# Performance work log

Hardware: AMD Instinct MI355X
Metric: run time of the kernel (lower is better)

Reference implementation:

```python
import jax, jax.numpy as jnp
import numpy as np

D = 1024      # d_model
H = 16        # n_head
DH = D // H   # d_head = 64
DFF = 4 * D   # 4096
B, T = 1, 4096
EPS = 1e-5


def _layernorm(x, scale, bias):
    mu = jnp.mean(x, axis=-1, keepdims=True)
    var = jnp.mean(jnp.square(x - mu), axis=-1, keepdims=True)
    return (x - mu) * jax.lax.rsqrt(var + EPS) * scale + bias


def setup_inputs() -> dict:
    key = jax.random.key(0)
    ks = jax.random.split(key, 8)
    s = 0.02
    return {
        "x": jax.random.normal(ks[0], (B, T, D), jnp.float32),
        "ln1_scale": jnp.ones((D,), jnp.float32),
        "ln1_bias": jnp.zeros((D,), jnp.float32),
        "W_attn": jax.random.normal(ks[1], (D, 3 * D), jnp.float32) * s,
        "b_attn": jnp.zeros((3 * D,), jnp.float32),
        "W_proj": jax.random.normal(ks[2], (D, D), jnp.float32) * s,
        "b_proj": jnp.zeros((D,), jnp.float32),
        "ln2_scale": jnp.ones((D,), jnp.float32),
        "ln2_bias": jnp.zeros((D,), jnp.float32),
        "W_fc": jax.random.normal(ks[3], (D, DFF), jnp.float32) * s,
        "b_fc": jnp.zeros((DFF,), jnp.float32),
        "W_fc2": jax.random.normal(ks[4], (DFF, D), jnp.float32) * s,
        "b_fc2": jnp.zeros((D,), jnp.float32),
    }


def reference(x, ln1_scale, ln1_bias, W_attn, b_attn, W_proj, b_proj,
              ln2_scale, ln2_bias, W_fc, b_fc, W_fc2, b_fc2):
    Bx, Tx, C = x.shape
    # --- attention branch ---
    h = _layernorm(x, ln1_scale, ln1_bias)
    qkv = h @ W_attn + b_attn                      # [B,T,3D]
    q, k, v = jnp.split(qkv, 3, axis=-1)
    q = q.reshape(Bx, Tx, H, DH).transpose(0, 2, 1, 3)  # [B,H,T,dh]
    k = k.reshape(Bx, Tx, H, DH).transpose(0, 2, 1, 3)
    v = v.reshape(Bx, Tx, H, DH).transpose(0, 2, 1, 3)
    att = jnp.einsum('bhqd,bhkd->bhqk', q, k) * (1.0 / jnp.sqrt(DH))
    causal = jnp.tril(jnp.ones((Tx, Tx), dtype=jnp.bool_))[None, None]
    att = jnp.where(causal, att, -jnp.inf)
    att = jax.nn.softmax(att, axis=-1)
    y = jnp.einsum('bhqk,bhkd->bhqd', att, v)      # [B,H,T,dh]
    y = y.transpose(0, 2, 1, 3).reshape(Bx, Tx, C)
    y = y @ W_proj + b_proj
    x = x + y
    # --- MLP branch ---
    h2 = _layernorm(x, ln2_scale, ln2_bias)
    m = jax.nn.gelu(h2 @ W_fc + b_fc)              # approximate gelu (flax default)
    m = m @ W_fc2 + b_fc2
    return x + m
```

## Files before the change

### kernel.cpp

```cpp
#include <hip/hip_runtime.h>
#include <hip/hip_bf16.h>

typedef short bf16x8 __attribute__((ext_vector_type(8)));
typedef float f32x4 __attribute__((ext_vector_type(4)));
typedef unsigned short u16;
typedef unsigned int u32;

#define TSEQ 4096
#define DMODEL 1024
#define NHEAD 16
#define DHEAD 64
#define DFF 4096

__device__ __forceinline__ u16 f2bf(float f) {
    u32 u = __builtin_bit_cast(u32, f);
    u32 lsb = (u >> 16) & 1u;
    u += 0x7fffu + lsb;
    return (u16)(u >> 16);
}

__device__ __forceinline__ float exp2_hw(float x) {
    float r;
    asm("v_exp_f32 %0, %1" : "=v"(r) : "v"(x));
    return r;
}

__device__ __forceinline__ float rcp_hw(float x) {
    float r;
    asm("v_rcp_f32 %0, %1" : "=v"(r) : "v"(x));
    return r;
}

__device__ __forceinline__ u32 cvt_pk_bf16(float a, float b) {
    u32 r;
    asm("v_cvt_pk_bf16_f32 %0, %1, %2" : "=v"(r) : "v"(a), "v"(b));
    return r;
}

__device__ __forceinline__ void gload_lds16(const u16* g, u16* l) {
    __builtin_amdgcn_global_load_lds(
        (const __attribute__((address_space(1))) u32*)g,
        (__attribute__((address_space(3))) u32*)l, 16, 0, 0);
}

__global__ __launch_bounds__(256)
void transpose_cast_kernel(const float* __restrict__ W, u16* __restrict__ Wt, int K, int N)
{
    __shared__ float tile[64][65];
    const int t = threadIdx.x;
    const int c = t & 63, r4 = t >> 6;
    const int col0 = blockIdx.x * 64;
    const int row0 = blockIdx.y * 64;
#pragma unroll
    for (int p = 0; p < 16; p++) {
        const int r = 4 * p + r4;
        tile[r][c] = W[(size_t)(row0 + r) * N + col0 + c];
    }
    __syncthreads();
#pragma unroll
    for (int p = 0; p < 16; p++) {
        const int r = 4 * p + r4;
        Wt[(size_t)(col0 + r) * K + row0 + c] = f2bf(tile[c][r]);
    }
}

__global__ __launch_bounds__(256)
void v_transpose_kernel(const u16* __restrict__ qkv, u16* __restrict__ Vtg)
{
    __shared__ u16 tile[64][72];
    const int t = threadIdx.x;
    const int hh = blockIdx.y, t0 = blockIdx.x * 64;
#pragma unroll
    for (int p = 0; p < 2; p++) {
        const int L = p * 2048 + t * 8;
        const int r = L >> 6, c = L & 63;
        const bf16x8 v = *(const bf16x8*)(qkv + (size_t)(t0 + r) * 3072 + 2048 + hh * 64 + c);
#pragma unroll
        for (int i = 0; i < 8; i++) tile[c + i][r] = (u16)v[i];
    }
    __syncthreads();
#pragma unroll
    for (int p = 0; p < 2; p++) {
        const int L = p * 2048 + t * 8;
        const int d = L >> 6, c = L & 63;
        bf16x8 v;
#pragma unroll
        for (int i = 0; i < 8; i++) v[i] = (short)tile[d][c + i];
        *(bf16x8*)(Vtg + (size_t)(hh * 64 + d) * TSEQ + t0 + c) = v;
    }
}

__global__ __launch_bounds__(256)
void ln_kernel(const float* __restrict__ x, const float* __restrict__ sc,
               const float* __restrict__ bi, u16* __restrict__ out)
{
    const int lane = threadIdx.x & 63;
    const int row = blockIdx.x * 4 + (threadIdx.x >> 6);
    const float* xr = x + (size_t)row * DMODEL;
    float4 v[4];
    float s = 0.f, s2 = 0.f;
#pragma unroll
    for (int q = 0; q < 4; q++) {
        v[q] = *(const float4*)(xr + 4 * (lane + 64 * q));
        s  += v[q].x + v[q].y + v[q].z + v[q].w;
        s2 += v[q].x * v[q].x + v[q].y * v[q].y + v[q].z * v[q].z + v[q].w * v[q].w;
    }
#pragma unroll
    for (int off = 1; off < 64; off <<= 1) {
        s  += __shfl_xor(s, off);
        s2 += __shfl_xor(s2, off);
    }
    const float mu = s * (1.f / DMODEL);
    const float rstd = rsqrtf(s2 * (1.f / DMODEL) - mu * mu + 1e-5f);
#pragma unroll
    for (int q = 0; q < 4; q++) {
        const int c = 4 * (lane + 64 * q);
        const float4 scv = *(const float4*)(sc + c);
        const float4 biv = *(const float4*)(bi + c);
        ushort4 ov;
        ov.x = f2bf((v[q].x - mu) * rstd * scv.x + biv.x);
        ov.y = f2bf((v[q].y - mu) * rstd * scv.y + biv.y);
        ov.z = f2bf((v[q].z - mu) * rstd * scv.z + biv.z);
        ov.w = f2bf((v[q].w - mu) * rstd * scv.w + biv.w);
        *(ushort4*)(out + (size_t)row * DMODEL + c) = ov;
    }
}

template<int BN, int GELU_F, int OUT_BF16, int HAS_RES, int HAS_BIAS, int FUSE_Z1 = 0>
__global__ __launch_bounds__(256)
void gemm_kernel(const u16* __restrict__ A, int lda,
                 const u16* __restrict__ Bt, int ldb,
                 const float* __restrict__ bias, const float* __restrict__ res,
                 u16* __restrict__ outb, float* __restrict__ outf0,
                 float* __restrict__ outf1, int M, int N, int Kblk)
{
    constexpr int MI = (BN == 128) ? 4 : 2;
    __shared__ u16 Alds[128 * 64];
    __shared__ u16 Blds[BN * 64];
    const int t = threadIdx.x;
    const int lane = t & 63, w = t >> 6;
    const int g = lane >> 4, fr = lane & 15;
    const int m0 = blockIdx.y * 128, n0 = blockIdx.x * BN;
    const size_t koff = (size_t)blockIdx.z * Kblk;
    const int rowbase = (BN == 128) ? (w >> 1) * 64 : w * 32;
    const int colbase = (BN == 128) ? (w & 1) * 64 : 0;
    float* outf = blockIdx.z ? outf1 : outf0;

    f32x4 zero4 = {0.f, 0.f, 0.f, 0.f};
    f32x4 acc[MI][4];
#pragma unroll
    for (int i = 0; i < MI; i++)
#pragma unroll
        for (int j = 0; j < 4; j++) acc[i][j] = zero4;

    for (int k0 = 0; k0 < Kblk; k0 += 64) {
        __syncthreads();
#pragma unroll
        for (int p = 0; p < 4; p++) {
            const int c = p * 256 + t;
            const int r = c >> 3, j = (c & 7) ^ (r & 7);
            gload_lds16(A + (size_t)(m0 + r) * lda + koff + k0 + j * 8, Alds + c * 8);
        }
#pragma unroll
        for (int p = 0; p < (BN == 128 ? 4 : 2); p++) {
            const int c = p * 256 + t;
            const int r = c >> 3, j = (c & 7) ^ (r & 7);
            gload_lds16(Bt + (size_t)(n0 + r) * ldb + koff + k0 + j * 8, Blds + c * 8);
        }
        __syncthreads();

#pragma unroll
        for (int ks = 0; ks < 2; ks++) {
            bf16x8 af[MI], bfr[4];
#pragma unroll
            for (int i = 0; i < MI; i++)
                af[i] = *(const bf16x8*)(Alds + (rowbase + i * 16 + fr) * 64 + (((ks * 4 + g) ^ (fr & 7)) * 8));
#pragma unroll
            for (int j = 0; j < 4; j++)
                bfr[j] = *(const bf16x8*)(Blds + (colbase + j * 16 + fr) * 64 + (((ks * 4 + g) ^ (fr & 7)) * 8));
#pragma unroll
            for (int i = 0; i < MI; i++)
#pragma unroll
                for (int j = 0; j < 4; j++)
                    acc[i][j] = __builtin_amdgcn_mfma_f32_16x16x32_bf16(af[i], bfr[j], acc[i][j], 0, 0, 0);
        }
    }

    const bool fuse = FUSE_Z1 && (blockIdx.z == 1);
#pragma unroll
    for (int j = 0; j < 4; j++) {
        const int col = n0 + colbase + j * 16 + fr;
        float bv = 0.f;
        if (HAS_BIAS) bv = bias[col];
        if (FUSE_Z1 && fuse) bv = bias[col];
#pragma unroll
        for (int i = 0; i < MI; i++) {
#pragma unroll
            for (int r = 0; r < 4; r++) {
                const int row = m0 + rowbase + i * 16 + g * 4 + r;
                float v = acc[i][j][r] + bv;
                if (GELU_F) {
                    const float q = 0.7978845608028654f * (v + 0.044715f * v * v * v);
                    const float e = exp2_hw(fminf(q, 30.f) * 2.8853900817779268f);
                    v = v * e * rcp_hw(e + 1.0f);
                }
                if (HAS_RES) v += res[(size_t)row * N + col];
                if (FUSE_Z1 && fuse) v += res[(size_t)row * N + col];
                if (OUT_BF16) outb[(size_t)row * N + col] = f2bf(v);
                else          outf[(size_t)row * N + col] = v;
            }
        }
    }
}

__global__ __launch_bounds__(256)
void fc2_merge_kernel(float* __restrict__ out, const float* __restrict__ part)
{
    const int i = blockIdx.x * 256 + threadIdx.x;
    const float4 o = ((const float4*)out)[i];
    const float4 p = ((const float4*)part)[i];
    float4 v;
    v.x = o.x + p.x;
    v.y = o.y + p.y;
    v.z = o.z + p.z;
    v.w = o.w + p.w;
    ((float4*)out)[i] = v;
}

__device__ __forceinline__ void softmax_update(
    const f32x4 st[4], bool diag, int klim, int g, int fr,
    float& mrow, float& lrow, f32x4 o[4], u16* Pl)
{
    const float ninf = -__builtin_inff();
    const float C = 0.125f * 1.4426950408889634f;
    float av[4][4];
#pragma unroll
    for (int ct = 0; ct < 4; ct++)
#pragma unroll
        for (int r = 0; r < 4; r++) {
            float aa = st[ct][r];
            if (diag && (ct * 16 + g * 4 + r) > klim) aa = ninf;
            av[ct][r] = aa;
        }
    float m0 = fmaxf(fmaxf(av[0][0], av[0][1]), fmaxf(av[0][2], av[0][3]));
    float m1 = fmaxf(fmaxf(av[1][0], av[1][1]), fmaxf(av[1][2], av[1][3]));
    float m2 = fmaxf(fmaxf(av[2][0], av[2][1]), fmaxf(av[2][2], av[2][3]));
    float m3 = fmaxf(fmaxf(av[3][0], av[3][1]), fmaxf(av[3][2], av[3][3]));
    float vm = fmaxf(fmaxf(m0, m1), fmaxf(m2, m3));
    vm = fmaxf(vm, __shfl_xor(vm, 16));
    vm = fmaxf(vm, __shfl_xor(vm, 32));
    const float mn = (vm <= mrow + 64.f) ? mrow : vm;
    const float mnC = mn * C;
    float rs = 0.f;
#pragma unroll
    for (int ct = 0; ct < 4; ct++) {
        const float p0 = exp2_hw(__builtin_fmaf(av[ct][0], C, -mnC));
        const float p1 = exp2_hw(__builtin_fmaf(av[ct][1], C, -mnC));
        const float p2 = exp2_hw(__builtin_fmaf(av[ct][2], C, -mnC));
        const float p3 = exp2_hw(__builtin_fmaf(av[ct][3], C, -mnC));
        rs += (p0 + p1) + (p2 + p3);
        uint2 pk;
        pk.x = cvt_pk_bf16(p0, p1);
        pk.y = cvt_pk_bf16(p2, p3);
        const int chunk = ct * 2 + (g >> 1);
        const int addr = fr * 64 + ((chunk ^ (fr & 7)) * 8) + (g & 1) * 4;
        *(uint2*)(Pl + addr) = pk;
    }
    rs += __shfl_xor(rs, 16);
    rs += __shfl_xor(rs, 32);
    const float sc = exp2_hw((mrow - mn) * C);
    lrow = __builtin_fmaf(lrow, sc, rs);
    const bool nores = (mn == mrow);
    mrow = mn;
    if (!__all(nores)) {
        float scb[4];
#pragma unroll
        for (int j = 0; j < 4; j++) scb[j] = __shfl(sc, g * 4 + j);
#pragma unroll
        for (int dt = 0; dt < 4; dt++)
#pragma unroll
            for (int j = 0; j < 4; j++) o[dt][j] *= scb[j];
    }
}

__global__ __launch_bounds__(512, 4)
void attn_kernel(const u16* __restrict__ qkv, const u16* __restrict__ Vtg,
                 u16* __restrict__ y)
{
    __shared__ u16 Klds[2][128 * 64];
    __shared__ u16 Vlds[2][64 * 128];
    __shared__ u16 Plds[8][16 * 64];
    const int t = threadIdx.x, lane = t & 63, w = t >> 6;
    const int g = lane >> 4, fr = lane & 15;
    const int wv = w & 3, grp = w >> 2;
    const int hh = blockIdx.y;
    const int ii = blockIdx.x;
    const int ntB = 64 - ii;
    const int qAw = ii * 64 + wv * 16;
    const int qBw = (63 - ii) * 64 + wv * 16;

    bf16x8 aqA[2], aqB[2];
#pragma unroll
    for (int s = 0; s < 2; s++) {
        aqA[s] = *(const bf16x8*)(qkv + (size_t)(qAw + fr) * 3072 + hh * 64 + s * 32 + g * 8);
        aqB[s] = *(const bf16x8*)(qkv + (size_t)(qBw + fr) * 3072 + hh * 64 + s * 32 + g * 8);
    }

    f32x4 zero4 = {0.f, 0.f, 0.f, 0.f};
    f32x4 oA[4] = {zero4, zero4, zero4, zero4};
    f32x4 oB[4] = {zero4, zero4, zero4, zero4};
    const float ninf = -__builtin_inff();
    float mA = ninf, lA = 0.f, mB = ninf, lB = 0.f;

    const int cK0 = t, cK1 = t + 512;
    const int rK0 = cK0 >> 3, jK0 = (cK0 & 7) ^ (rK0 & 7);
    const int rK1 = cK1 >> 3, jK1 = (cK1 & 7) ^ (rK1 & 7);
    const int rv0 = cK0 >> 4, cj0 = cK0 & 15;
    const int jv0 = (cj0 & 8) | ((cj0 & 7) ^ (rv0 & 7));
    const int rv1 = cK1 >> 4, cj1 = cK1 & 15;
    const int jv1 = (cj1 & 8) | ((cj1 & 7) ^ (rv1 & 7));
    const u16* gk0 = qkv + (size_t)rK0 * 3072 + 1024 + hh * 64 + jK0 * 8;
    const u16* gk1 = qkv + (size_t)rK1 * 3072 + 1024 + hh * 64 + jK1 * 8;
    const u16* gv0 = Vtg + (size_t)(hh * 64 + rv0) * TSEQ + jv0 * 8;
    const u16* gv1 = Vtg + (size_t)(hh * 64 + rv1) * TSEQ + jv1 * 8;

#define STAGE(buf, k0) do { \
        gload_lds16(gk0 + (size_t)(k0) * 3072, Klds[buf] + cK0 * 8); \
        gload_lds16(gk1 + (size_t)(k0) * 3072, Klds[buf] + cK1 * 8); \
        gload_lds16(gv0 + (k0), Vlds[buf] + cK0 * 8); \
        gload_lds16(gv1 + (k0), Vlds[buf] + cK1 * 8); \
    } while (0)

    const int nIter = (65 - ii) >> 1;
    STAGE(0, 0);

    int cur = 0;
    for (int j = 0; j < nIter; j++) {
        __syncthreads();
        if (j + 1 < nIter) STAGE(cur ^ 1, (j + 1) * 128);

        const int kt = 2 * j + grp;
        const bool aB = kt < ntB;
        const bool aA = kt <= ii;
        if (aB | aA) {
            const u16* Kl = Klds[cur] + grp * (64 * 64);
            const u16* Vl = Vlds[cur];
            const int klim = wv * 16 + fr;

            f32x4 stA[4] = {zero4, zero4, zero4, zero4};
            f32x4 stB[4] = {zero4, zero4, zero4, zero4};
#pragma unroll
            for (int ct = 0; ct < 4; ct++) {
#pragma unroll
                for (int ds = 0; ds < 2; ds++) {
                    const bf16x8 bk = *(const bf16x8*)(Kl + (ct * 16 + fr) * 64 + (((ds * 4 + g) ^ (fr & 7)) * 8));
                    if (aB) stB[ct] = __builtin_amdgcn_mfma_f32_16x16x32_bf16(bk, aqB[ds], stB[ct], 0, 0, 0);
                    if (aA) stA[ct] = __builtin_amdgcn_mfma_f32_16x16x32_bf16(bk, aqA[ds], stA[ct], 0, 0, 0);
                }
            }

            if (aB) {
                softmax_update(stB, kt == ntB - 1, klim, g, fr, mB, lB, oB, Plds[w]);
                __builtin_amdgcn_s_waitcnt(0xc07f);
#pragma unroll
                for (int kkh = 0; kkh < 2; kkh++) {
                    const bf16x8 pa = *(const bf16x8*)(&Plds[w][fr * 64 + (((kkh * 4 + g) ^ (fr & 7)) * 8)]);
#pragma unroll
                    for (int dt = 0; dt < 4; dt++) {
                        const int cc = grp * 8 + kkh * 4 + g;
                        const bf16x8 bv = *(const bf16x8*)(Vl + (dt * 16 + fr) * 128 + (((cc & 8) | ((cc & 7) ^ (fr & 7))) * 8));
                        oB[dt] = __builtin_amdgcn_mfma_f32_16x16x32_bf16(pa, bv, oB[dt], 0, 0, 0);
                    }
                }
            }
            if (aA) {
                softmax_update(stA, kt == ii, klim, g, fr, mA, lA, oA, Plds[w]);
                __builtin_amdgcn_s_waitcnt(0xc07f);
#pragma unroll
                for (int kkh = 0; kkh < 2; kkh++) {
                    const bf16x8 pa = *(const bf16x8*)(&Plds[w][fr * 64 + (((kkh * 4 + g) ^ (fr & 7)) * 8)]);
#pragma unroll
                    for (int dt = 0; dt < 4; dt++) {
                        const int cc = grp * 8 + kkh * 4 + g;
                        const bf16x8 bv = *(const bf16x8*)(Vl + (dt * 16 + fr) * 128 + (((cc & 8) | ((cc & 7) ^ (fr & 7))) * 8));
                        oA[dt] = __builtin_amdgcn_mfma_f32_16x16x32_bf16(pa, bv, oA[dt], 0, 0, 0);
                    }
                }
            }
        }
        cur ^= 1;
    }
#undef STAGE

    __syncthreads();
    float* Of = (float*)&Klds[0][0];
    float2* Ml = (float2*)&Vlds[0][0];
    const float C = 0.125f * 1.4426950408889634f;
    if (grp == 1) {
#pragma unroll
        for (int dt = 0; dt < 4; dt++)
#pragma unroll
            for (int jq = 0; jq < 4; jq++) {
                Of[((wv * 2 + 0) * 16 + g * 4 + jq) * 64 + dt * 16 + fr] = oA[dt][jq];
                Of[((wv * 2 + 1) * 16 + g * 4 + jq) * 64 + dt * 16 + fr] = oB[dt][jq];
            }
        if (g == 0) {
            Ml[(wv * 2 + 0) * 16 + fr] = make_float2(mA, lA);
            Ml[(wv * 2 + 1) * 16 + fr] = make_float2(mB, lB);
        }
    }
    __syncthreads();
    if (grp == 0) {
#pragma unroll
        for (int jq = 0; jq < 4; jq++) {
            {
                const float m0 = __shfl(mA, g * 4 + jq), l0 = __shfl(lA, g * 4 + jq);
                const float2 ml1 = Ml[(wv * 2 + 0) * 16 + g * 4 + jq];
                const float mm = fmaxf(m0, ml1.x);
                const float s0 = exp2_hw((m0 - mm) * C);
                const float s1 = exp2_hw((ml1.x - mm) * C);
                const float rl = rcp_hw(__builtin_fmaf(l0, s0, ml1.y * s1));
#pragma unroll
                for (int dt = 0; dt < 4; dt++) {
                    const float o1 = Of[((wv * 2 + 0) * 16 + g * 4 + jq) * 64 + dt * 16 + fr];
                    y[(size_t)(qAw + g * 4 + jq) * DMODEL + hh * 64 + dt * 16 + fr] =
                        f2bf((oA[dt][jq] * s0 + o1 * s1) * rl);
                }
            }
            {
                const float m0 = __shfl(mB, g * 4 + jq), l0 = __shfl(lB, g * 4 + jq);
                const float2 ml1 = Ml[(wv * 2 + 1) * 16 + g * 4 + jq];
                const float mm = fmaxf(m0, ml1.x);
                const float s0 = exp2_hw((m0 - mm) * C);
                const float s1 = exp2_hw((ml1.x - mm) * C);
                const float rl = rcp_hw(__builtin_fmaf(l0, s0, ml1.y * s1));
#pragma unroll
                for (int dt = 0; dt < 4; dt++) {
                    const float o1 = Of[((wv * 2 + 1) * 16 + g * 4 + jq) * 64 + dt * 16 + fr];
                    y[(size_t)(qBw + g * 4 + jq) * DMODEL + hh * 64 + dt * 16 + fr] =
                        f2bf((oB[dt][jq] * s0 + o1 * s1) * rl);
                }
            }
        }
    }
}

extern "C" void kernel_launch(void* const* d_in, const int* in_sizes, int n_in,
                              void* d_out, int out_size, void* d_ws, size_t ws_size,
                              hipStream_t stream)
{
    const float* x      = (const float*)d_in[0];
    const float* ln1_s  = (const float*)d_in[1];
    const float* ln1_b  = (const float*)d_in[2];
    const float* W_attn = (const float*)d_in[3];
    const float* b_attn = (const float*)d_in[4];
    const float* W_proj = (const float*)d_in[5];
    const float* b_proj = (const float*)d_in[6];
    const float* ln2_s  = (const float*)d_in[7];
    const float* ln2_b  = (const float*)d_in[8];
    const float* W_fc   = (const float*)d_in[9];
    const float* b_fc   = (const float*)d_in[10];
    const float* W_fc2  = (const float*)d_in[11];
    const float* b_fc2  = (const float*)d_in[12];
    float* out = (float*)d_out;

    char* ws = (char*)d_ws;
    u16* WtAttn = (u16*)ws; ws += (size_t)3072 * 1024 * 2;
    u16* WtProj = (u16*)ws; ws += (size_t)1024 * 1024 * 2;
    u16* WtFc   = (u16*)ws; ws += (size_t)4096 * 1024 * 2;
    u16* WtFc2  = (u16*)ws; ws += (size_t)1024 * 4096 * 2;
    u16* bufA   = (u16*)ws; ws += (size_t)4096 * 1024 * 2;
    u16* bufB   = (u16*)ws; ws += (size_t)4096 * 4096 * 2;
    float* x1   = (float*)ws; ws += (size_t)4096 * 1024 * 4;
    u16* Vtg    = (u16*)x1;
    float* P0   = (float*)d_ws;

    transpose_cast_kernel<<<dim3(3072 / 64, 1024 / 64), 256, 0, stream>>>(W_attn, WtAttn, 1024, 3072);
    transpose_cast_kernel<<<dim3(1024 / 64, 1024 / 64), 256, 0, stream>>>(W_proj, WtProj, 1024, 1024);
    transpose_cast_kernel<<<dim3(4096 / 64, 1024 / 64), 256, 0, stream>>>(W_fc,   WtFc,   1024, 4096);
    transpose_cast_kernel<<<dim3(1024 / 64, 4096 / 64), 256, 0, stream>>>(W_fc2,  WtFc2,  4096, 1024);

    ln_kernel<<<TSEQ / 4, 256, 0, stream>>>(x, ln1_s, ln1_b, bufA);
    gemm_kernel<128, 0, 1, 0, 1><<<dim3(24, 32, 1), 256, 0, stream>>>(
        bufA, 1024, WtAttn, 1024, b_attn, nullptr, bufB, nullptr, nullptr, 4096, 3072, 1024);
    v_transpose_kernel<<<dim3(TSEQ / 64, NHEAD), 256, 0, stream>>>(bufB, Vtg);
    attn_kernel<<<dim3(32, NHEAD), 512, 0, stream>>>(bufB, Vtg, bufA);
    gemm_kernel<64, 0, 0, 1, 1><<<dim3(16, 32, 1), 256, 0, stream>>>(
        bufA, 1024, WtProj, 1024, b_proj, x, nullptr, x1, nullptr, 4096, 1024, 1024);

    ln_kernel<<<TSEQ / 4, 256, 0, stream>>>(x1, ln2_s, ln2_b, bufA);
    gemm_kernel<128, 1, 1, 0, 1><<<dim3(32, 32, 1), 256, 0, stream>>>(
        bufA, 1024, WtFc, 1024, b_fc, nullptr, bufB, nullptr, nullptr, 4096, 4096, 1024);
    gemm_kernel<128, 0, 0, 0, 0, 1><<<dim3(8, 32, 2), 256, 0, stream>>>(
        bufB, 4096, WtFc2, 4096, b_fc2, x1, nullptr, P0, out, 4096, 1024, 2048);
    fc2_merge_kernel<<<4096, 256, 0, stream>>>(out, P0);
}
```

Measured before the change: 298.5 us.

## Merge weight casts and LN1 into one prep kernel; add 256x128 FC GEMM

Combines the four weight transpose/cast launches and the first layernorm into a single prep kernel that dispatches on block index, removing launch overhead and serialization between small kernels. Adds a new 512-thread GEMM with a 256x128 output tile for the FC+GELU layer, which raises data reuse per block and halves the block count. The new GEMM has no double buffering, so load latency may be less hidden, and the larger tile can lower occupancy.

```diff
diff --git a/kernel.cpp b/kernel.cpp
--- a/kernel.cpp
+++ b/kernel.cpp
@@ -43,14 +43,14 @@
         (__attribute__((address_space(3))) u32*)l, 16, 0, 0);
 }
 
-__global__ __launch_bounds__(256)
-void transpose_cast_kernel(const float* __restrict__ W, u16* __restrict__ Wt, int K, int N)
-{
-    __shared__ float tile[64][65];
+__device__ __forceinline__ void transpose_tile(
+    const float* __restrict__ W, u16* __restrict__ Wt, int K, int N, int bx, int by,
+    float (*tile)[65])
+{
     const int t = threadIdx.x;
     const int c = t & 63, r4 = t >> 6;
-    const int col0 = blockIdx.x * 64;
-    const int row0 = blockIdx.y * 64;
+    const int col0 = bx * 64;
+    const int row0 = by * 64;
 #pragma unroll
     for (int p = 0; p < 16; p++) {
         const int r = 4 * p + r4;
@@ -64,38 +64,12 @@
     }
 }
 
-__global__ __launch_bounds__(256)
-void v_transpose_kernel(const u16* __restrict__ qkv, u16* __restrict__ Vtg)
-{
-    __shared__ u16 tile[64][72];
-    const int t = threadIdx.x;
-    const int hh = blockIdx.y, t0 = blockIdx.x * 64;
-#pragma unroll
-    for (int p = 0; p < 2; p++) {
-        const int L = p * 2048 + t * 8;
-        const int r = L >> 6, c = L & 63;
-        const bf16x8 v = *(const bf16x8*)(qkv + (size_t)(t0 + r) * 3072 + 2048 + hh * 64 + c);
-#pragma unroll
-        for (int i = 0; i < 8; i++) tile[c + i][r] = (u16)v[i];
-    }
-    __syncthreads();
-#pragma unroll
-    for (int p = 0; p < 2; p++) {
-        const int L = p * 2048 + t * 8;
-        const int d = L >> 6, c = L & 63;
-        bf16x8 v;
-#pragma unroll
-        for (int i = 0; i < 8; i++) v[i] = (short)tile[d][c + i];
-        *(bf16x8*)(Vtg + (size_t)(hh * 64 + d) * TSEQ + t0 + c) = v;
-    }
-}
-
-__global__ __launch_bounds__(256)
-void ln_kernel(const float* __restrict__ x, const float* __restrict__ sc,
-               const float* __restrict__ bi, u16* __restrict__ out)
+__device__ __forceinline__ void ln_rows(
+    const float* __restrict__ x, const float* __restrict__ sc,
+    const float* __restrict__ bi, u16* __restrict__ out, int blk)
 {
     const int lane = threadIdx.x & 63;
-    const int row = blockIdx.x * 4 + (threadIdx.x >> 6);
+    const int row = blk * 4 + (threadIdx.x >> 6);
     const float* xr = x + (size_t)row * DMODEL;
     float4 v[4];
     float s = 0.f, s2 = 0.f;
@@ -124,6 +98,60 @@
         ov.w = f2bf((v[q].w - mu) * rstd * scv.w + biv.w);
         *(ushort4*)(out + (size_t)row * DMODEL + c) = ov;
     }
+}
+
+__global__ __launch_bounds__(256)
+void prep_kernel(const float* __restrict__ x, const float* __restrict__ ln1_s,
+                 const float* __restrict__ ln1_b, u16* __restrict__ h,
+                 const float* __restrict__ W_attn, u16* __restrict__ WtAttn,
+                 const float* __restrict__ W_proj, u16* __restrict__ WtProj,
+                 const float* __restrict__ W_fc,   u16* __restrict__ WtFc,
+                 const float* __restrict__ W_fc2,  u16* __restrict__ WtFc2)
+{
+    __shared__ float tile[64][65];
+    int b = blockIdx.x;
+    if (b < 1024) { ln_rows(x, ln1_s, ln1_b, h, b); return; }
+    b -= 1024;
+    if (b < 768)  { transpose_tile(W_attn, WtAttn, 1024, 3072, b % 48, b / 48, tile); return; }
+    b -= 768;
+    if (b < 256)  { transpose_tile(W_proj, WtProj, 1024, 1024, b % 16, b / 16, tile); return; }
+    b -= 256;
+    if (b < 1024) { transpose_tile(W_fc,   WtFc,   1024, 4096, b % 64, b / 64, tile); return; }
+    b -= 1024;
+    transpose_tile(W_fc2, WtFc2, 4096, 1024, b % 16, b / 16, tile);
+}
+
+__global__ __launch_bounds__(256)
+void v_transpose_kernel(const u16* __restrict__ qkv, u16* __restrict__ Vtg)
+{
+    __shared__ u16 tile[64][72];
+    const int t = threadIdx.x;
+    const int hh = blockIdx.y, t0 = blockIdx.x * 64;
+#pragma unroll
+    for (int p = 0; p < 2; p++) {
+        const int L = p * 2048 + t * 8;
+        const int r = L >> 6, c = L & 63;
+        const bf16x8 v = *(const bf16x8*)(qkv + (size_t)(t0 + r) * 3072 + 2048 + hh * 64 + c);
+#pragma unroll
+        for (int i = 0; i < 8; i++) tile[c + i][r] = (u16)v[i];
+    }
+    __syncthreads();
+#pragma unroll
+    for (int p = 0; p < 2; p++) {
+        const int L = p * 2048 + t * 8;
+        const int d = L >> 6, c = L & 63;
+        bf16x8 v;
+#pragma unroll
+        for (int i = 0; i < 8; i++) v[i] = (short)tile[d][c + i];
+        *(bf16x8*)(Vtg + (size_t)(hh * 64 + d) * TSEQ + t0 + c) = v;
+    }
+}
+
+__global__ __launch_bounds__(256)
+void ln_kernel(const float* __restrict__ x, const float* __restrict__ sc,
+               const float* __restrict__ bi, u16* __restrict__ out)
+{
+    ln_rows(x, sc, bi, out, blockIdx.x);
 }
 
 template<int BN, int GELU_F, int OUT_BF16, int HAS_RES, int HAS_BIAS, int FUSE_Z1 = 0>
@@ -208,6 +236,79 @@
                 if (FUSE_Z1 && fuse) v += res[(size_t)row * N + col];
                 if (OUT_BF16) outb[(size_t)row * N + col] = f2bf(v);
                 else          outf[(size_t)row * N + col] = v;
+            }
+        }
+    }
+}
+
+__global__ __launch_bounds__(512, 2)
+void gemm256_kernel(const u16* __restrict__ A, const u16* __restrict__ Bt,
+                    const float* __restrict__ bias, u16* __restrict__ outb,
+                    int M, int N, int K)
+{
+    __shared__ u16 Alds[256 * 64];
+    __shared__ u16 Blds[128 * 64];
+    const int t = threadIdx.x;
+    const int lane = t & 63, w = t >> 6;
+    const int g = lane >> 4, fr = lane & 15;
+    const int m0 = blockIdx.y * 256, n0 = blockIdx.x * 128;
+    const int rowbase = (w >> 1) * 64;
+    const int colbase = (w & 1) * 64;
+
+    f32x4 zero4 = {0.f, 0.f, 0.f, 0.f};
+    f32x4 acc[4][4];
+#pragma unroll
+    for (int i = 0; i < 4; i++)
+#pragma unroll
+        for (int j = 0; j < 4; j++) acc[i][j] = zero4;
+
+    for (int k0 = 0; k0 < K; k0 += 64) {
+        __syncthreads();
+#pragma unroll
+        for (int p = 0; p < 4; p++) {
+            const int c = p * 512 + t;
+            const int r = c >> 3, j = (c & 7) ^ (r & 7);
+            gload_lds16(A + (size_t)(m0 + r) * K + k0 + j * 8, Alds + c * 8);
+        }
+#pragma unroll
+        for (int p = 0; p < 2; p++) {
+            const int c = p * 512 + t;
+            const int r = c >> 3, j = (c & 7) ^ (r & 7);
+            gload_lds16(Bt + (size_t)(n0 + r) * K + k0 + j * 8, Blds + c * 8);
+        }
+        __syncthreads();
+
+#pragma unroll
+        for (int ks = 0; ks < 2; ks++) {
+            bf16x8 af[4], bfr[4];
+#pragma unroll
+            for (int i = 0; i < 4; i++)
+                af[i] = *(const bf16x8*)(Alds + (rowbase + i * 16 + fr) * 64 + (((ks * 4 + g) ^ (fr & 7)) * 8));
+#pragma unroll
+            for (int j = 0; j < 4; j++)
+                bfr[j] = *(const bf16x8*)(Blds + (colbase + j * 16 + fr) * 64 + (((ks * 4 + g) ^ (fr & 7)) * 8));
+#pragma unroll
+            for (int i = 0; i < 4; i++)
+#pragma unroll
+                for (int j = 0; j < 4; j++)
+                    acc[i][j] = __builtin_amdgcn_mfma_f32_16x16x32_bf16(af[i], bfr[j], acc[i][j], 0, 0, 0);
+        }
+    }
+
+#pragma unroll
+    for (int j = 0; j < 4; j++) {
+        const int col = n0 + colbase + j * 16 + fr;
+        const float bv = bias[col];
+#pragma unroll
+        for (int i = 0; i < 4; i++) {
+#pragma unroll
+            for (int r = 0; r < 4; r++) {
+                const int row = m0 + rowbase + i * 16 + g * 4 + r;
+                float v = acc[i][j][r] + bv;
+                const float q = 0.7978845608028654f * (v + 0.044715f * v * v * v);
+                const float e = exp2_hw(fminf(q, 30.f) * 2.8853900817779268f);
+                v = v * e * rcp_hw(e + 1.0f);
+                outb[(size_t)row * N + col] = f2bf(v);
             }
         }
     }
@@ -475,12 +576,10 @@
     u16* Vtg    = (u16*)x1;
     float* P0   = (float*)d_ws;
 
-    transpose_cast_kernel<<<dim3(3072 / 64, 1024 / 64), 256, 0, stream>>>(W_attn, WtAttn, 1024, 3072);
-    transpose_cast_kernel<<<dim3(1024 / 64, 1024 / 64), 256, 0, stream>>>(W_proj, WtProj, 1024, 1024);
-    transpose_cast_kernel<<<dim3(4096 / 64, 1024 / 64), 256, 0, stream>>>(W_fc,   WtFc,   1024, 4096);
-    transpose_cast_kernel<<<dim3(1024 / 64, 4096 / 64), 256, 0, stream>>>(W_fc2,  WtFc2,  4096, 1024);
-
-    ln_kernel<<<TSEQ / 4, 256, 0, stream>>>(x, ln1_s, ln1_b, bufA);
+    prep_kernel<<<4096, 256, 0, stream>>>(x, ln1_s, ln1_b, bufA,
+                                          W_attn, WtAttn, W_proj, WtProj,
+                                          W_fc, WtFc, W_fc2, WtFc2);
+
     gemm_kernel<128, 0, 1, 0, 1><<<dim3(24, 32, 1), 256, 0, stream>>>(
         bufA, 1024, WtAttn, 1024, b_attn, nullptr, bufB, nullptr, nullptr, 4096, 3072, 1024);
     v_transpose_kernel<<<dim3(TSEQ / 64, NHEAD), 256, 0, stream>>>(bufB, Vtg);
@@ -489,8 +588,8 @@
         bufA, 1024, WtProj, 1024, b_proj, x, nullptr, x1, nullptr, 4096, 1024, 1024);
 
     ln_kernel<<<TSEQ / 4, 256, 0, stream>>>(x1, ln2_s, ln2_b, bufA);
-    gemm_kernel<128, 1, 1, 0, 1><<<dim3(32, 32, 1), 256, 0, stream>>>(
-        bufA, 1024, WtFc, 1024, b_fc, nullptr, bufB, nullptr, nullptr, 4096, 4096, 1024);
+    gemm256_kernel<<<dim3(32, 16), 512, 0, stream>>>(
+        bufA, WtFc, b_fc, bufB, 4096, 4096, 1024);
     gemm_kernel<128, 0, 0, 0, 0, 1><<<dim3(8, 32, 2), 256, 0, stream>>>(
         bufB, 4096, WtFc2, 4096, b_fc2, x1, nullptr, P0, out, 4096, 1024, 2048);
     fc2_merge_kernel<<<4096, 256, 0, stream>>>(out, P0);
```

Result: faster. 280.9 us (-5.9%).
